# Performance work log

Hardware: AMD Instinct MI355X
Metric: run time of the kernel (lower is better)

## Reference

```python
import jax, jax.numpy as jnp
import numpy as np

N_NODES = 100000
N_EDGES = 1600000
NFEATS, NHIDS, NOUT = 128, 128, 64


def _gcn_conv(x, W, b, src, dst, n_nodes):
    # PyG GCNConv: linear transform, then symmetric-normalized aggregation
    # over A + I (self-loops added), then bias.
    h = x @ W                                        # [N, out]
    loop = jnp.arange(n_nodes, dtype=src.dtype)
    s = jnp.concatenate([src, loop])                 # [E + N]
    d = jnp.concatenate([dst, loop])                 # [E + N]
    deg = jax.ops.segment_sum(jnp.ones_like(d, dtype=h.dtype), d,
                              num_segments=n_nodes)  # degree of A + I
    dinv = jnp.where(deg > 0, jax.lax.rsqrt(deg), 0.0)
    norm = dinv[s] * dinv[d]                         # [E + N]
    msg = h[s] * norm[:, None]                       # gather + scale
    out = jax.ops.segment_sum(msg, d, num_segments=n_nodes)  # scatter-add
    return out + b


def setup_inputs() -> dict:
    key = jax.random.key(0)
    k1, k2, k3, k4 = jax.random.split(key, 4)
    edge_index = jax.random.randint(k1, (2, N_EDGES), 0, N_NODES, dtype=jnp.int64)
    x = jax.random.normal(k2, (N_NODES, NFEATS), dtype=jnp.float32)
    W1 = jax.random.normal(k3, (NFEATS, NHIDS), dtype=jnp.float32) / np.sqrt(NFEATS)
    b1 = jnp.zeros((NHIDS,), dtype=jnp.float32)
    W2 = jax.random.normal(k4, (NHIDS, NOUT), dtype=jnp.float32) / np.sqrt(NHIDS)
    b2 = jnp.zeros((NOUT,), dtype=jnp.float32)
    return {"edge_index": edge_index, "x": x, "W1": W1, "b1": b1,
            "W2": W2, "b2": b2}


def reference(edge_index, x, W1, b1, W2, b2):
    src, dst = edge_index[0], edge_index[1]
    n = x.shape[0]
    h = jax.nn.relu(_gcn_conv(x, W1, b1, src, dst, n))
    # dropout(p=0.5, train=False) is the identity in eval mode
    out = _gcn_conv(h, W2, b2, src, dst, n)
    return out
```

## Files before the change

kernel.cpp:

```cpp
#include <hip/hip_runtime.h>
#include <cstdint>
#include <cstddef>

#define NFEATS 128
#define NHIDS  128
#define NOUT   64
#define SB     256
#define CHUNK  4096

using bf16x8 = __attribute__((ext_vector_type(8))) short;
using f32x4  = __attribute__((ext_vector_type(4))) float;
using u32x4  = __attribute__((ext_vector_type(4))) unsigned int;

__device__ inline unsigned short f2bf(float f) {
    union { float f; unsigned int u; } v; v.f = f;
    unsigned int r = (v.u + 0x7FFFu + ((v.u >> 16) & 1u)) >> 16;
    return (unsigned short)r;
}
__device__ inline float bflo(unsigned int u) { return __uint_as_float(u << 16); }
__device__ inline float bfhi(unsigned int u) { return __uint_as_float(u & 0xFFFF0000u); }

__global__ void detect_wpack(const void* __restrict__ p, int* __restrict__ flag,
                             long long n_nodes,
                             const float* __restrict__ W1, unsigned short* __restrict__ Wf1,
                             const float* __restrict__ W2, unsigned short* __restrict__ Wf2) {
    if (blockIdx.x == 0) {
        if (threadIdx.x < 64) {
            const long long* q = (const long long*)p;
            long long v = q[threadIdx.x];
            int bad = (v < 0 || v >= n_nodes) ? 1 : 0;
            unsigned long long m = __ballot(bad);
            if (threadIdx.x == 0) *flag = (m != 0ULL) ? 1 : 0;
        }
        return;
    }
    int i = (blockIdx.x - 1) * 256 + threadIdx.x;
    if (i < 128 * 128) {
        int k = i >> 7, n = i & 127;
        Wf1[(((k >> 3) * 128) + n) * 8 + (k & 7)] = f2bf(W1[i]);
    }
    if (i < 128 * 64) {
        int k = i >> 6, n = i & 63;
        Wf2[(((k >> 3) * 64) + n) * 8 + (k & 7)] = f2bf(W2[i]);
    }
}

__global__ __launch_bounds__(512)
void hist_kernel(const void* __restrict__ edges, const int* __restrict__ flag,
                 int* __restrict__ histT, int ne, int nch, int nbkt) {
    __shared__ int h[1024];
    int c = blockIdx.x, t = threadIdx.x;
    for (int i = t; i < nbkt; i += 512) h[i] = 0;
    __syncthreads();
    int beg = c * CHUNK, end = min(ne, beg + CHUNK);
    bool is32 = (*flag != 0);
    for (int i = beg + t; i < end; i += 512) {
        int d = is32 ? ((const int*)edges)[ne + i]
                     : (int)((const long long*)edges)[ne + i];
        atomicAdd(&h[d >> 8], 1);
    }
    __syncthreads();
    for (int i = t; i < nbkt; i += 512)
        histT[i * nch + c] = h[i];
}

__global__ void scan_block(const int* __restrict__ v, int* __restrict__ incl,
                           int* __restrict__ partial, int n) {
    __shared__ int sh[256];
    int t = threadIdx.x;
    int i = blockIdx.x * 256 + t;
    sh[t] = (i < n) ? v[i] : 0;
    __syncthreads();
    for (int off = 1; off < 256; off <<= 1) {
        int add = (t >= off) ? sh[t - off] : 0;
        __syncthreads();
        sh[t] += add;
        __syncthreads();
    }
    if (i < n) incl[i] = sh[t];
    if (t == 255) partial[blockIdx.x] = sh[255];
}

__global__ void scan_partials(int* partial, int nb) {
    __shared__ int sh[512];
    __shared__ int carry;
    int t = threadIdx.x;
    if (t == 0) carry = 0;
    __syncthreads();
    for (int base = 0; base < nb; base += 512) {
        int idx = base + t;
        sh[t] = (idx < nb) ? partial[idx] : 0;
        __syncthreads();
        for (int off = 1; off < 512; off <<= 1) {
            int add = (t >= off) ? sh[t - off] : 0;
            __syncthreads();
            sh[t] += add;
            __syncthreads();
        }
        int excl = carry + ((t == 0) ? 0 : sh[t - 1]);
        if (idx < nb) partial[idx] = excl;
        __syncthreads();
        if (t == 0) carry += sh[511];
        __syncthreads();
    }
}

__global__ __launch_bounds__(512)
void scatter_chunks(const void* __restrict__ edges, const int* __restrict__ flag,
                    const int* __restrict__ histT, const int* __restrict__ incl,
                    const int* __restrict__ partial,
                    unsigned int* __restrict__ ebuf,
                    int ne, int nch, int nbkt) {
    __shared__ int cnt[512];
    __shared__ int cursor[512];
    __shared__ int delta[512];
    __shared__ unsigned int   srt[CHUNK];
    __shared__ unsigned short bkl[CHUNK];
    int c = blockIdx.x, t = threadIdx.x;
    if (t < nbkt) cnt[t] = 0;
    int cb = 0;
    if (t < nbkt) {
        int idx = t * nch + c;
        cb = partial[idx >> 8] + incl[idx] - histT[idx];
    }
    __syncthreads();

    int beg = c * CHUNK, end = min(ne, beg + CHUNK);
    int nloc = end - beg;
    bool is32 = (*flag != 0);

    unsigned int rec[8];
    int bk[8];
#pragma unroll
    for (int r = 0; r < 8; ++r) {
        int i = beg + t + r * 512;
        bk[r] = -1;
        if (i < end) {
            int s, d;
            if (is32) {
                s = ((const int*)edges)[i];
                d = ((const int*)edges)[ne + i];
            } else {
                s = (int)((const long long*)edges)[i];
                d = (int)((const long long*)edges)[ne + i];
            }
            rec[r] = ((unsigned int)s << 8) | (unsigned int)(d & (SB - 1));
            bk[r]  = d >> 8;
            atomicAdd(&cnt[bk[r]], 1);
        }
    }
    __syncthreads();

    int v0 = (t < nbkt) ? cnt[t] : 0;
    cursor[t] = v0;
    __syncthreads();
    for (int off = 1; off < 512; off <<= 1) {
        int add = (t >= off) ? cursor[t - off] : 0;
        __syncthreads();
        cursor[t] += add;
        __syncthreads();
    }
    int inc = cursor[t];
    __syncthreads();
    int lb = inc - v0;
    cursor[t] = lb;
    if (t < nbkt) delta[t] = cb - lb;
    __syncthreads();

#pragma unroll
    for (int r = 0; r < 8; ++r) {
        if (bk[r] >= 0) {
            int pos = atomicAdd(&cursor[bk[r]], 1);
            srt[pos] = rec[r];
            bkl[pos] = (unsigned short)bk[r];
        }
    }
    __syncthreads();

    for (int i = t; i < nloc; i += 512)
        ebuf[delta[bkl[i]] + i] = srt[i];
}

__global__ void bucket_finalize(const unsigned int* __restrict__ ebuf,
                                const int* __restrict__ histT, const int* __restrict__ inclG,
                                const int* __restrict__ partial,
                                int* __restrict__ row_ptr, float* __restrict__ dinv,
                                int* __restrict__ csr_src,
                                int n, int e, int nch, int nbkt) {
    __shared__ int deg[SB];
    __shared__ int incl[SB];
    __shared__ int cur[SB];
    __shared__ int stage[4608];
    __shared__ int sbase, sbend;
    int b = blockIdx.x, t = threadIdx.x;
    int node0 = b * SB;
    int nn = min(SB, n - node0);
    if (t == 0) {
        int i0 = b * nch;
        sbase = partial[i0 >> 8] + inclG[i0] - histT[i0];
        if (b == nbkt - 1) sbend = e;
        else {
            int i1 = (b + 1) * nch;
            sbend = partial[i1 >> 8] + inclG[i1] - histT[i1];
        }
    }
    deg[t] = 0;
    __syncthreads();
    int base = sbase, bend = sbend;

    for (int i = base + t; i < bend; i += SB)
        atomicAdd(&deg[ebuf[i] & (SB - 1)], 1);
    __syncthreads();

    incl[t] = deg[t];
    __syncthreads();
    for (int off = 1; off < SB; off <<= 1) {
        int add = (t >= off) ? incl[t - off] : 0;
        __syncthreads();
        incl[t] += add;
        __syncthreads();
    }
    int lrow = base + incl[t] - deg[t];
    cur[t] = lrow - base;
    if (t < nn) {
        row_ptr[node0 + t] = lrow;
        dinv[node0 + t]    = rsqrtf((float)(deg[t] + 1));
    }
    if (b == nbkt - 1 && t == 0) row_ptr[n] = e;
    __syncthreads();

    int cntE = bend - base;
    if (cntE <= 4608) {
        for (int i = base + t; i < bend; i += SB) {
            unsigned int r = ebuf[i];
            int pos = atomicAdd(&cur[r & (SB - 1)], 1);
            stage[pos] = (int)(r >> 8);
        }
        __syncthreads();
        for (int i = t; i < cntE; i += SB)
            csr_src[base + i] = stage[i];
    } else {
        for (int i = base + t; i < bend; i += SB) {
            unsigned int r = ebuf[i];
            int pos = atomicAdd(&cur[r & (SB - 1)], 1);
            csr_src[base + pos] = (int)(r >> 8);
        }
    }
}

template <int NC, bool F32IN>
__launch_bounds__(256)
__global__ void gemm_mfma(const void* __restrict__ Xin,
                          const unsigned short* __restrict__ Wf,
                          const float* __restrict__ dinv,
                          unsigned short* __restrict__ hs, int nrows) {
    constexpr int K = 128;
    __shared__ __align__(16) unsigned short Xl[16 * 128 * 8];

    const int tid  = threadIdx.x;
    const int row0 = blockIdx.x * 128;

    for (int i = tid; i < 128 * 32; i += 256) {
        int r  = i >> 5;
        int c4 = i & 31;
        int gr = row0 + r;
        ushort4 v = make_ushort4(0, 0, 0, 0);
        if (gr < nrows) {
            if (F32IN) {
                float4 f = ((const float4*)((const float*)Xin + (size_t)gr * K))[c4];
                v.x = f2bf(f.x); v.y = f2bf(f.y); v.z = f2bf(f.z); v.w = f2bf(f.w);
            } else {
                v = ((const ushort4*)((const unsigned short*)Xin + (size_t)gr * K))[c4];
            }
        }
        int k   = c4 * 4;
        int grp = k >> 3;
        int j0  = k & 7;
        *(ushort4*)(Xl + ((size_t)grp * 128 + r) * 8 + j0) = v;
    }
    __syncthreads();

    const int wv   = tid >> 6;
    const int lane = tid & 63;
    const int m    = lane & 15;
    const int q    = lane >> 4;

    bf16x8 af[2][4];
#pragma unroll
    for (int h = 0; h < 2; ++h)
#pragma unroll
        for (int kt = 0; kt < 4; ++kt)
            af[h][kt] = *(const bf16x8*)(Xl + (((kt * 4 + q) * 128) + h * 64 + wv * 16 + m) * 8);

    int   rbase[2];
    float dv[2][4];
#pragma unroll
    for (int h = 0; h < 2; ++h) {
        rbase[h] = row0 + h * 64 + wv * 16 + q * 4;
#pragma unroll
        for (int i = 0; i < 4; ++i)
            dv[h][i] = (rbase[h] + i < nrows) ? dinv[rbase[h] + i] : 0.f;
    }

#pragma unroll
    for (int nt = 0; nt < NC / 16; ++nt) {
        bf16x8 bfr[4];
#pragma unroll
        for (int kt = 0; kt < 4; ++kt)
            bfr[kt] = *(const bf16x8*)(Wf + (((size_t)(kt * 4 + q) * NC) + nt * 16 + m) * 8);
#pragma unroll
        for (int h = 0; h < 2; ++h) {
            f32x4 acc = {0.f, 0.f, 0.f, 0.f};
#pragma unroll
            for (int kt = 0; kt < 4; ++kt)
                acc = __builtin_amdgcn_mfma_f32_16x16x32_bf16(af[h][kt], bfr[kt], acc, 0, 0, 0);
#pragma unroll
            for (int i = 0; i < 4; ++i) {
                int g = rbase[h] + i;
                if (g < nrows)
                    hs[(size_t)g * NC + nt * 16 + m] = f2bf(acc[i] * dv[h][i]);
            }
        }
    }
}

__launch_bounds__(256)
__global__ void aggregate_fused_l1(const int* __restrict__ row_ptr,
                                   const int* __restrict__ csr_src,
                                   const uint4* __restrict__ hsu,
                                   const float* __restrict__ dinv,
                                   const float* __restrict__ b,
                                   const unsigned short* __restrict__ Wf2,
                                   unsigned short* __restrict__ hs2, int n) {
    constexpr int TPN = 16;
    constexpr int NPB = 16;
    constexpr int CH  = 16;

    __shared__ __align__(16) unsigned short h1t[16 * 136];
    __shared__ float dl[16];
    __shared__ __align__(16) unsigned short outt[16 * 64];

    const int node0 = blockIdx.x * NPB;
    const int nl    = threadIdx.x / TPN;
    const int t     = threadIdx.x % TPN;
    const int node  = min(node0 + nl, n - 1);
    const int lane  = threadIdx.x & 63;
    const int gb    = lane & ~(TPN - 1);

    uint4 u = hsu[(size_t)node * TPN + t];
    float a[8];
    a[0] = bflo(u.x); a[1] = bfhi(u.x); a[2] = bflo(u.y); a[3] = bfhi(u.y);
    a[4] = bflo(u.z); a[5] = bfhi(u.z); a[6] = bflo(u.w); a[7] = bfhi(u.w);

    int beg = row_ptr[node], end = row_ptr[node + 1];

    if (beg < end) {
        const u32x4* hb = (const u32x4*)hsu;
        u32x4 v[CH];
        int sva;
        int base = beg;

        {
            const int* pc0 = csr_src + min(base + t, end - 1);
            asm volatile("global_load_dword %0, %1, off" : "=&v"(sva) : "v"(pc0));
        }
        asm volatile("s_waitcnt vmcnt(0)");
        __builtin_amdgcn_sched_barrier(0);

        while (true) {
            int rem = min(CH, end - base);

#pragma unroll
            for (int j = 0; j < CH; ++j) {
                int jj = min(j, rem - 1);
                int sj = __shfl(sva, gb + jj, 64);
                const u32x4* p = hb + (size_t)sj * TPN + t;
                asm volatile("global_load_dwordx4 %0, %1, off" : "=&v"(v[j]) : "v"(p));
            }

            int  nbase = base + CH;
            bool more  = nbase < end;
            if (more) {
                const int* pc0 = csr_src + min(nbase + t, end - 1);
                asm volatile("global_load_dword %0, %1, off" : "=&v"(sva) : "v"(pc0));
                asm volatile("s_waitcnt vmcnt(1)");
            } else {
                asm volatile("s_waitcnt vmcnt(0)");
            }
            __builtin_amdgcn_sched_barrier(0);

#pragma unroll
            for (int j = 0; j < CH; ++j) {
                if (j < rem) {
                    unsigned int x0 = v[j][0], x1 = v[j][1], x2 = v[j][2], x3 = v[j][3];
                    a[0] += bflo(x0); a[1] += bfhi(x0);
                    a[2] += bflo(x1); a[3] += bfhi(x1);
                    a[4] += bflo(x2); a[5] += bfhi(x2);
                    a[6] += bflo(x3); a[7] += bfhi(x3);
                }
            }

            if (!more) break;
            base = nbase;
            asm volatile("s_waitcnt vmcnt(0)");
            __builtin_amdgcn_sched_barrier(0);
        }
    }

    float dvn = dinv[node];
    float4 b0 = ((const float4*)b)[2 * t];
    float4 b1 = ((const float4*)b)[2 * t + 1];
    float o[8];
    o[0] = a[0] * dvn + b0.x; o[1] = a[1] * dvn + b0.y;
    o[2] = a[2] * dvn + b0.z; o[3] = a[3] * dvn + b0.w;
    o[4] = a[4] * dvn + b1.x; o[5] = a[5] * dvn + b1.y;
    o[6] = a[6] * dvn + b1.z; o[7] = a[7] * dvn + b1.w;
#pragma unroll
    for (int j = 0; j < 8; ++j) o[j] = fmaxf(o[j], 0.f);

    uint4 ov;
    ov.x = (unsigned int)f2bf(o[0]) | ((unsigned int)f2bf(o[1]) << 16);
    ov.y = (unsigned int)f2bf(o[2]) | ((unsigned int)f2bf(o[3]) << 16);
    ov.z = (unsigned int)f2bf(o[4]) | ((unsigned int)f2bf(o[5]) << 16);
    ov.w = (unsigned int)f2bf(o[6]) | ((unsigned int)f2bf(o[7]) << 16);
    *(uint4*)((char*)h1t + (size_t)nl * 272 + t * 16) = ov;
    if (t == 0) dl[nl] = dvn;
    __syncthreads();

    {
        const int wv = threadIdx.x >> 6;
        const int m  = lane & 15;
        const int q  = lane >> 4;

        f32x4 acc = {0.f, 0.f, 0.f, 0.f};
#pragma unroll
        for (int kt = 0; kt < 4; ++kt) {
            bf16x8 af  = *(const bf16x8*)((const char*)h1t + (size_t)m * 272 + q * 16 + kt * 64);
            bf16x8 bfr = *(const bf16x8*)(Wf2 + (((size_t)(kt * 4 + q) * 64) + wv * 16 + m) * 8);
            acc = __builtin_amdgcn_mfma_f32_16x16x32_bf16(af, bfr, acc, 0, 0, 0);
        }
#pragma unroll
        for (int i = 0; i < 4; ++i) {
            int nd = q * 4 + i;
            outt[nd * 64 + wv * 16 + m] = f2bf(acc[i] * dl[nd]);
        }
    }
    __syncthreads();

    {
        int i = threadIdx.x;
        if (i < 128) {
            int gnode = node0 + (i >> 3);
            if (gnode < n)
                ((uint4*)hs2)[(size_t)gnode * 8 + (i & 7)] = ((const uint4*)outt)[i];
        }
    }
}

template <int F, bool RELU, bool OUTBF>
__launch_bounds__(256)
__global__ void aggregate_bf16(const int* __restrict__ row_ptr,
                               const int* __restrict__ csr_src,
                               const uint4* __restrict__ hsu,
                               const float* __restrict__ dinv,
                               const float* __restrict__ b,
                               void* __restrict__ out, int n) {
    constexpr int TPN  = F / 8;
    constexpr int NPB  = 256 / TPN;
    constexpr int CH   = 16;
    constexpr int NCSR = CH / TPN;
    int node = blockIdx.x * NPB + threadIdx.x / TPN;
    int t    = threadIdx.x % TPN;
    if (node >= n) return;
    const int lane = threadIdx.x & 63;
    const int gb   = lane & ~(TPN - 1);

    uint4 u = hsu[(size_t)node * TPN + t];
    float a[8];
    a[0] = bflo(u.x); a[1] = bfhi(u.x); a[2] = bflo(u.y); a[3] = bfhi(u.y);
    a[4] = bflo(u.z); a[5] = bfhi(u.z); a[6] = bflo(u.w); a[7] = bfhi(u.w);

    int beg = row_ptr[node], end = row_ptr[node + 1];

    if (beg < end) {
        const u32x4* hb = (const u32x4*)hsu;
        u32x4 v[CH];
        int sva, svb;
        int base = beg;

        {
            const int* pc0 = csr_src + min(base + t, end - 1);
            asm volatile("global_load_dword %0, %1, off" : "=&v"(sva) : "v"(pc0));
            if (NCSR == 2) {
                const int* pc1 = csr_src + min(base + TPN + t, end - 1);
                asm volatile("global_load_dword %0, %1, off" : "=&v"(svb) : "v"(pc1));
            }
        }
        asm volatile("s_waitcnt vmcnt(0)");
        __builtin_amdgcn_sched_barrier(0);

        while (true) {
            int rem = min(CH, end - base);

#pragma unroll
            for (int j = 0; j < CH; ++j) {
                int jj = min(j, rem - 1);
                int sj;
                if (TPN == 16) {
                    sj = __shfl(sva, gb + jj, 64);
                } else {
                    int s0 = __shfl(sva, gb + (jj & 7), 64);
                    int s1 = __shfl(svb, gb + (jj & 7), 64);
                    sj = (jj < 8) ? s0 : s1;
                }
                const u32x4* p = hb + (size_t)sj * TPN + t;
                asm volatile("global_load_dwordx4 %0, %1, off" : "=&v"(v[j]) : "v"(p));
            }

            int  nbase = base + CH;
            bool more  = nbase < end;
            if (more) {
                const int* pc0 = csr_src + min(nbase + t, end - 1);
                asm volatile("global_load_dword %0, %1, off" : "=&v"(sva) : "v"(pc0));
                if (NCSR == 2) {
                    const int* pc1 = csr_src + min(nbase + TPN + t, end - 1);
                    asm volatile("global_load_dword %0, %1, off" : "=&v"(svb) : "v"(pc1));
                }
                if (NCSR == 1) asm volatile("s_waitcnt vmcnt(1)");
                else           asm volatile("s_waitcnt vmcnt(2)");
            } else {
                asm volatile("s_waitcnt vmcnt(0)");
            }
            __builtin_amdgcn_sched_barrier(0);

#pragma unroll
            for (int j = 0; j < CH; ++j) {
                if (j < rem) {
                    unsigned int x0 = v[j][0], x1 = v[j][1], x2 = v[j][2], x3 = v[j][3];
                    a[0] += bflo(x0); a[1] += bfhi(x0);
                    a[2] += bflo(x1); a[3] += bfhi(x1);
                    a[4] += bflo(x2); a[5] += bfhi(x2);
                    a[6] += bflo(x3); a[7] += bfhi(x3);
                }
            }

            if (!more) break;
            base = nbase;
            asm volatile("s_waitcnt vmcnt(0)");
            __builtin_amdgcn_sched_barrier(0);
        }
    }

    float dvn = dinv[node];
    float4 b0 = ((const float4*)b)[2 * t];
    float4 b1 = ((const float4*)b)[2 * t + 1];
    float o[8];
    o[0] = a[0] * dvn + b0.x; o[1] = a[1] * dvn + b0.y;
    o[2] = a[2] * dvn + b0.z; o[3] = a[3] * dvn + b0.w;
    o[4] = a[4] * dvn + b1.x; o[5] = a[5] * dvn + b1.y;
    o[6] = a[6] * dvn + b1.z; o[7] = a[7] * dvn + b1.w;
    if (RELU) {
#pragma unroll
        for (int j = 0; j < 8; ++j) o[j] = fmaxf(o[j], 0.f);
    }
    if (OUTBF) {
        uint4 ov;
        ov.x = (unsigned int)f2bf(o[0]) | ((unsigned int)f2bf(o[1]) << 16);
        ov.y = (unsigned int)f2bf(o[2]) | ((unsigned int)f2bf(o[3]) << 16);
        ov.z = (unsigned int)f2bf(o[4]) | ((unsigned int)f2bf(o[5]) << 16);
        ov.w = (unsigned int)f2bf(o[6]) | ((unsigned int)f2bf(o[7]) << 16);
        ((uint4*)out)[(size_t)node * TPN + t] = ov;
    } else {
        float4* op = (float4*)out + (size_t)node * (F / 4) + 2 * t;
        op[0] = make_float4(o[0], o[1], o[2], o[3]);
        op[1] = make_float4(o[4], o[5], o[6], o[7]);
    }
}

extern "C" void kernel_launch(void* const* d_in, const int* in_sizes, int n_in,
                              void* d_out, int out_size, void* d_ws, size_t ws_size,
                              hipStream_t stream) {
    const void*  edge = d_in[0];
    const float* x    = (const float*)d_in[1];
    const float* W1   = (const float*)d_in[2];
    const float* b1   = (const float*)d_in[3];
    const float* W2   = (const float*)d_in[4];
    const float* b2   = (const float*)d_in[5];
    float* out = (float*)d_out;

    const int E    = in_sizes[0] / 2;
    const int N    = in_sizes[1] / NFEATS;
    const int NBKT = (N + SB - 1) / SB;
    const int NCH  = (E + CHUNK - 1) / CHUNK;
    const int M    = NBKT * NCH;

    char* w = (char*)d_ws;
    auto carve = [&](size_t bytes) { void* p = w; w += (bytes + 255) & ~(size_t)255; return p; };
    int*            flag       = (int*)           carve(256);
    int*            histT      = (int*)           carve(sizeof(int) * (size_t)M);
    int*            incl       = (int*)           carve(sizeof(int) * (size_t)M);
    int*            partial    = (int*)           carve(sizeof(int) * 4096);
    int*            row_ptr    = (int*)           carve(sizeof(int) * ((size_t)N + 1));
    float*          dinv       = (float*)         carve(sizeof(float) * (size_t)N);
    unsigned int*   ebuf       = (unsigned int*)  carve(sizeof(int) * (size_t)E);
    int*            csr_src    = (int*)           carve(sizeof(int) * (size_t)E);
    unsigned short* Wf1        = (unsigned short*)carve(2 * (size_t)NFEATS * NHIDS);
    unsigned short* Wf2        = (unsigned short*)carve(2 * (size_t)NHIDS * NOUT);
    unsigned short* hs1        = (unsigned short*)carve(2 * (size_t)N * NHIDS);
    unsigned short* hs2        = (unsigned short*)carve(2 * (size_t)N * NOUT);

    const int nbS = (M + 255) / 256;

    detect_wpack<<<65, 256, 0, stream>>>(edge, flag, (long long)N, W1, Wf1, W2, Wf2);

    hist_kernel<<<NCH, 512, 0, stream>>>(edge, flag, histT, E, NCH, NBKT);
    scan_block<<<nbS, 256, 0, stream>>>(histT, incl, partial, M);
    scan_partials<<<1, 512, 0, stream>>>(partial, nbS);
    scatter_chunks<<<NCH, 512, 0, stream>>>(edge, flag, histT, incl, partial,
                                            ebuf, E, NCH, NBKT);
    bucket_finalize<<<NBKT, SB, 0, stream>>>(ebuf, histT, incl, partial,
                                             row_ptr, dinv, csr_src, N, E, NCH, NBKT);

    gemm_mfma<NHIDS, true><<<(N + 127) / 128, 256, 0, stream>>>(x, Wf1, dinv, hs1, N);

    aggregate_fused_l1<<<(N + 15) / 16, 256, 0, stream>>>(
        row_ptr, csr_src, (const uint4*)hs1, dinv, b1, Wf2, hs2, N);

    {
        constexpr int NPB = 256 / (NOUT / 8);
        aggregate_bf16<NOUT, false, false><<<(N + NPB - 1) / NPB, 256, 0, stream>>>(
            row_ptr, csr_src, (const uint4*)hs2, dinv, b2, out, N);
    }
}
```

Baseline: 248.8 us.

## Compute degrees early and fuse layer-1 GEMM into the edge scatter launch

Degrees are now counted with global atomics in the histogram kernel, and dinv is computed alongside the partial scan. The layer-1 GEMM therefore no longer waits on bucket_finalize and runs as extra blocks of the scatter kernel, so the compute-bound GEMM can overlap the memory-bound scatter and one launch is removed. In exchange the histogram pays 1.6M global atomics on deg, and the GEMM tile is reshaped to 512-thread blocks that each handle 128 rows with one 16-row fragment per wave.

```diff
diff --git a/kernel.cpp b/kernel.cpp
--- a/kernel.cpp
+++ b/kernel.cpp
@@ -23,7 +23,8 @@
 __global__ void detect_wpack(const void* __restrict__ p, int* __restrict__ flag,
                              long long n_nodes,
                              const float* __restrict__ W1, unsigned short* __restrict__ Wf1,
-                             const float* __restrict__ W2, unsigned short* __restrict__ Wf2) {
+                             const float* __restrict__ W2, unsigned short* __restrict__ Wf2,
+                             int* __restrict__ deg, int n) {
     if (blockIdx.x == 0) {
         if (threadIdx.x < 64) {
             const long long* q = (const long long*)p;
@@ -36,18 +37,21 @@
     }
     int i = (blockIdx.x - 1) * 256 + threadIdx.x;
     if (i < 128 * 128) {
-        int k = i >> 7, n = i & 127;
-        Wf1[(((k >> 3) * 128) + n) * 8 + (k & 7)] = f2bf(W1[i]);
+        int k = i >> 7, n2 = i & 127;
+        Wf1[(((k >> 3) * 128) + n2) * 8 + (k & 7)] = f2bf(W1[i]);
     }
     if (i < 128 * 64) {
-        int k = i >> 6, n = i & 63;
-        Wf2[(((k >> 3) * 64) + n) * 8 + (k & 7)] = f2bf(W2[i]);
-    }
+        int k = i >> 6, n2 = i & 63;
+        Wf2[(((k >> 3) * 64) + n2) * 8 + (k & 7)] = f2bf(W2[i]);
+    }
+    for (int j = i; j < n; j += 64 * 256)
+        deg[j] = 0;
 }
 
 __global__ __launch_bounds__(512)
 void hist_kernel(const void* __restrict__ edges, const int* __restrict__ flag,
-                 int* __restrict__ histT, int ne, int nch, int nbkt) {
+                 int* __restrict__ histT, int* __restrict__ deg,
+                 int ne, int nch, int nbkt) {
     __shared__ int h[1024];
     int c = blockIdx.x, t = threadIdx.x;
     for (int i = t; i < nbkt; i += 512) h[i] = 0;
@@ -58,6 +62,7 @@
         int d = is32 ? ((const int*)edges)[ne + i]
                      : (int)((const long long*)edges)[ne + i];
         atomicAdd(&h[d >> 8], 1);
+        atomicAdd(&deg[d], 1);
     }
     __syncthreads();
     for (int i = t; i < nbkt; i += 512)
@@ -81,7 +86,14 @@
     if (t == 255) partial[blockIdx.x] = sh[255];
 }
 
-__global__ void scan_partials(int* partial, int nb) {
+__global__ __launch_bounds__(512)
+void scan_partials_dinv(int* __restrict__ partial, int nb,
+                        const int* __restrict__ deg, float* __restrict__ dinv, int n) {
+    if (blockIdx.x != 0) {
+        int i = (blockIdx.x - 1) * 512 + threadIdx.x;
+        if (i < n) dinv[i] = rsqrtf((float)(deg[i] + 1));
+        return;
+    }
     __shared__ int sh[512];
     __shared__ int carry;
     int t = threadIdx.x;
@@ -105,17 +117,86 @@
     }
 }
 
+__device__ __forceinline__ void gemm_tile_512(const float* __restrict__ Xin,
+                                              const unsigned short* __restrict__ Wf,
+                                              const float* __restrict__ dinv,
+                                              unsigned short* __restrict__ hs,
+                                              int nrows, int row0, char* smem) {
+    constexpr int K = 128, NC = 128;
+    unsigned short* Xl = (unsigned short*)smem;
+
+    const int tid = threadIdx.x;
+    for (int i = tid; i < 128 * 32; i += 512) {
+        int r  = i >> 5;
+        int c4 = i & 31;
+        int gr = row0 + r;
+        ushort4 v = make_ushort4(0, 0, 0, 0);
+        if (gr < nrows) {
+            float4 f = ((const float4*)(Xin + (size_t)gr * K))[c4];
+            v.x = f2bf(f.x); v.y = f2bf(f.y); v.z = f2bf(f.z); v.w = f2bf(f.w);
+        }
+        int k   = c4 * 4;
+        int grp = k >> 3;
+        int j0  = k & 7;
+        *(ushort4*)(Xl + ((size_t)grp * 128 + r) * 8 + j0) = v;
+    }
+    __syncthreads();
+
+    const int wv   = tid >> 6;
+    const int lane = tid & 63;
+    const int m    = lane & 15;
+    const int q    = lane >> 4;
+
+    bf16x8 af[4];
+#pragma unroll
+    for (int kt = 0; kt < 4; ++kt)
+        af[kt] = *(const bf16x8*)(Xl + (((kt * 4 + q) * 128) + wv * 16 + m) * 8);
+
+    const int rbase = row0 + wv * 16 + q * 4;
+    float dv[4];
+#pragma unroll
+    for (int i = 0; i < 4; ++i)
+        dv[i] = (rbase + i < nrows) ? dinv[rbase + i] : 0.f;
+
+#pragma unroll
+    for (int nt = 0; nt < NC / 16; ++nt) {
+        bf16x8 bfr[4];
+#pragma unroll
+        for (int kt = 0; kt < 4; ++kt)
+            bfr[kt] = *(const bf16x8*)(Wf + (((size_t)(kt * 4 + q) * NC) + nt * 16 + m) * 8);
+        f32x4 acc = {0.f, 0.f, 0.f, 0.f};
+#pragma unroll
+        for (int kt = 0; kt < 4; ++kt)
+            acc = __builtin_amdgcn_mfma_f32_16x16x32_bf16(af[kt], bfr[kt], acc, 0, 0, 0);
+#pragma unroll
+        for (int i = 0; i < 4; ++i) {
+            int g = rbase + i;
+            if (g < nrows)
+                hs[(size_t)g * NC + nt * 16 + m] = f2bf(acc[i] * dv[i]);
+        }
+    }
+}
+
 __global__ __launch_bounds__(512)
-void scatter_chunks(const void* __restrict__ edges, const int* __restrict__ flag,
-                    const int* __restrict__ histT, const int* __restrict__ incl,
-                    const int* __restrict__ partial,
-                    unsigned int* __restrict__ ebuf,
-                    int ne, int nch, int nbkt) {
-    __shared__ int cnt[512];
-    __shared__ int cursor[512];
-    __shared__ int delta[512];
-    __shared__ unsigned int   srt[CHUNK];
-    __shared__ unsigned short bkl[CHUNK];
+void scatter_gemm(const void* __restrict__ edges, const int* __restrict__ flag,
+                  const int* __restrict__ histT, const int* __restrict__ incl,
+                  const int* __restrict__ partial,
+                  unsigned int* __restrict__ ebuf,
+                  int ne, int nch, int nbkt,
+                  const float* __restrict__ x, const unsigned short* __restrict__ Wf1,
+                  const float* __restrict__ dinv, unsigned short* __restrict__ hs1,
+                  int nrows) {
+    __shared__ __align__(16) char smem[32768];
+    if ((int)blockIdx.x >= nch) {
+        gemm_tile_512(x, Wf1, dinv, hs1, nrows, ((int)blockIdx.x - nch) * 128, smem);
+        return;
+    }
+    int*            cnt    = (int*)smem;
+    int*            cursor = (int*)(smem + 2048);
+    int*            delta  = (int*)(smem + 4096);
+    unsigned int*   srt    = (unsigned int*)(smem + 6144);
+    unsigned short* bkl    = (unsigned short*)(smem + 22528);
+
     int c = blockIdx.x, t = threadIdx.x;
     if (t < nbkt) cnt[t] = 0;
     int cb = 0;
@@ -184,7 +265,7 @@
 __global__ void bucket_finalize(const unsigned int* __restrict__ ebuf,
                                 const int* __restrict__ histT, const int* __restrict__ inclG,
                                 const int* __restrict__ partial,
-                                int* __restrict__ row_ptr, float* __restrict__ dinv,
+                                int* __restrict__ row_ptr,
                                 int* __restrict__ csr_src,
                                 int n, int e, int nch, int nbkt) {
     __shared__ int deg[SB];
@@ -222,10 +303,7 @@
     }
     int lrow = base + incl[t] - deg[t];
     cur[t] = lrow - base;
-    if (t < nn) {
-        row_ptr[node0 + t] = lrow;
-        dinv[node0 + t]    = rsqrtf((float)(deg[t] + 1));
-    }
+    if (t < nn) row_ptr[node0 + t] = lrow;
     if (b == nbkt - 1 && t == 0) row_ptr[n] = e;
     __syncthreads();
 
@@ -244,82 +322,6 @@
             unsigned int r = ebuf[i];
             int pos = atomicAdd(&cur[r & (SB - 1)], 1);
             csr_src[base + pos] = (int)(r >> 8);
-        }
-    }
-}
-
-template <int NC, bool F32IN>
-__launch_bounds__(256)
-__global__ void gemm_mfma(const void* __restrict__ Xin,
-                          const unsigned short* __restrict__ Wf,
-                          const float* __restrict__ dinv,
-                          unsigned short* __restrict__ hs, int nrows) {
-    constexpr int K = 128;
-    __shared__ __align__(16) unsigned short Xl[16 * 128 * 8];
-
-    const int tid  = threadIdx.x;
-    const int row0 = blockIdx.x * 128;
-
-    for (int i = tid; i < 128 * 32; i += 256) {
-        int r  = i >> 5;
-        int c4 = i & 31;
-        int gr = row0 + r;
-        ushort4 v = make_ushort4(0, 0, 0, 0);
-        if (gr < nrows) {
-            if (F32IN) {
-                float4 f = ((const float4*)((const float*)Xin + (size_t)gr * K))[c4];
-                v.x = f2bf(f.x); v.y = f2bf(f.y); v.z = f2bf(f.z); v.w = f2bf(f.w);
-            } else {
-                v = ((const ushort4*)((const unsigned short*)Xin + (size_t)gr * K))[c4];
-            }
-        }
-        int k   = c4 * 4;
-        int grp = k >> 3;
-        int j0  = k & 7;
-        *(ushort4*)(Xl + ((size_t)grp * 128 + r) * 8 + j0) = v;
-    }
-    __syncthreads();
-
-    const int wv   = tid >> 6;
-    const int lane = tid & 63;
-    const int m    = lane & 15;
-    const int q    = lane >> 4;
-
-    bf16x8 af[2][4];
-#pragma unroll
-    for (int h = 0; h < 2; ++h)
-#pragma unroll
-        for (int kt = 0; kt < 4; ++kt)
-            af[h][kt] = *(const bf16x8*)(Xl + (((kt * 4 + q) * 128) + h * 64 + wv * 16 + m) * 8);
-
-    int   rbase[2];
-    float dv[2][4];
-#pragma unroll
-    for (int h = 0; h < 2; ++h) {
-        rbase[h] = row0 + h * 64 + wv * 16 + q * 4;
-#pragma unroll
-        for (int i = 0; i < 4; ++i)
-            dv[h][i] = (rbase[h] + i < nrows) ? dinv[rbase[h] + i] : 0.f;
-    }
-
-#pragma unroll
-    for (int nt = 0; nt < NC / 16; ++nt) {
-        bf16x8 bfr[4];
-#pragma unroll
-        for (int kt = 0; kt < 4; ++kt)
-            bfr[kt] = *(const bf16x8*)(Wf + (((size_t)(kt * 4 + q) * NC) + nt * 16 + m) * 8);
-#pragma unroll
-        for (int h = 0; h < 2; ++h) {
-            f32x4 acc = {0.f, 0.f, 0.f, 0.f};
-#pragma unroll
-            for (int kt = 0; kt < 4; ++kt)
-                acc = __builtin_amdgcn_mfma_f32_16x16x32_bf16(af[h][kt], bfr[kt], acc, 0, 0, 0);
-#pragma unroll
-            for (int i = 0; i < 4; ++i) {
-                int g = rbase[h] + i;
-                if (g < nrows)
-                    hs[(size_t)g * NC + nt * 16 + m] = f2bf(acc[i] * dv[h][i]);
-            }
         }
     }
 }
@@ -601,6 +603,7 @@
     int*            incl       = (int*)           carve(sizeof(int) * (size_t)M);
     int*            partial    = (int*)           carve(sizeof(int) * 4096);
     int*            row_ptr    = (int*)           carve(sizeof(int) * ((size_t)N + 1));
+    int*            deg        = (int*)           carve(sizeof(int) * (size_t)N);
     float*          dinv       = (float*)         carve(sizeof(float) * (size_t)N);
     unsigned int*   ebuf       = (unsigned int*)  carve(sizeof(int) * (size_t)E);
     int*            csr_src    = (int*)           carve(sizeof(int) * (size_t)E);
@@ -610,18 +613,23 @@
     unsigned short* hs2        = (unsigned short*)carve(2 * (size_t)N * NOUT);
 
     const int nbS = (M + 255) / 256;
-
-    detect_wpack<<<65, 256, 0, stream>>>(edge, flag, (long long)N, W1, Wf1, W2, Wf2);
-
-    hist_kernel<<<NCH, 512, 0, stream>>>(edge, flag, histT, E, NCH, NBKT);
+    const int GB  = (N + 127) / 128;
+
+    detect_wpack<<<65, 256, 0, stream>>>(edge, flag, (long long)N, W1, Wf1, W2, Wf2,
+                                         deg, N);
+
+    hist_kernel<<<NCH, 512, 0, stream>>>(edge, flag, histT, deg, E, NCH, NBKT);
+
     scan_block<<<nbS, 256, 0, stream>>>(histT, incl, partial, M);
-    scan_partials<<<1, 512, 0, stream>>>(partial, nbS);
-    scatter_chunks<<<NCH, 512, 0, stream>>>(edge, flag, histT, incl, partial,
-                                            ebuf, E, NCH, NBKT);
+    scan_partials_dinv<<<1 + (N + 511) / 512, 512, 0, stream>>>(partial, nbS,
+                                                                deg, dinv, N);
+
+    scatter_gemm<<<NCH + GB, 512, 0, stream>>>(edge, flag, histT, incl, partial,
+                                               ebuf, E, NCH, NBKT,
+                                               x, Wf1, dinv, hs1, N);
+
     bucket_finalize<<<NBKT, SB, 0, stream>>>(ebuf, histT, incl, partial,
-                                             row_ptr, dinv, csr_src, N, E, NCH, NBKT);
-
-    gemm_mfma<NHIDS, true><<<(N + 127) / 128, 256, 0, stream>>>(x, Wf1, dinv, hs1, N);
+                                             row_ptr, csr_src, N, E, NCH, NBKT);
 
     aggregate_fused_l1<<<(N + 15) / 16, 256, 0, stream>>>(
         row_ptr, csr_src, (const uint4*)hs1, dinv, b1, Wf2, hs2, N);
```

New measurement: 298.1 us. 1.2x slower.

## Store layer-2 features in feature-sliced layout and aggregate one slice per thread

Applied to the files above, without the earlier changes.

The fused layer-1 kernel now writes hs2 as 8 slices of 16 bytes per node, each stored contiguously across nodes, so slice s of node v sits at s*n+v. The layer-2 aggregation becomes a new kernel with one thread per node per slice. Each thread loads its own CSR indices and gathers 16-byte rows from a single slice, and blocks are interleaved so that consecutive blocks cover the eight slices of the same node range. The goal is to shrink the gathered working set per slice so it stays in cache, and to drop the cross-lane shuffles. In exchange, each thread now re-reads the CSR index list (eight times as many index loads) and does more serial per-thread work on high-degree nodes, which can cause imbalance within a wave.

```diff
diff --git a/kernel.cpp b/kernel.cpp
--- a/kernel.cpp
+++ b/kernel.cpp
@@ -36,12 +36,12 @@
     }
     int i = (blockIdx.x - 1) * 256 + threadIdx.x;
     if (i < 128 * 128) {
-        int k = i >> 7, n = i & 127;
-        Wf1[(((k >> 3) * 128) + n) * 8 + (k & 7)] = f2bf(W1[i]);
+        int k = i >> 7, n2 = i & 127;
+        Wf1[(((k >> 3) * 128) + n2) * 8 + (k & 7)] = f2bf(W1[i]);
     }
     if (i < 128 * 64) {
-        int k = i >> 6, n = i & 63;
-        Wf2[(((k >> 3) * 64) + n) * 8 + (k & 7)] = f2bf(W2[i]);
+        int k = i >> 6, n2 = i & 63;
+        Wf2[(((k >> 3) * 64) + n2) * 8 + (k & 7)] = f2bf(W2[i]);
     }
 }
 
@@ -450,97 +450,78 @@
     {
         int i = threadIdx.x;
         if (i < 128) {
-            int gnode = node0 + (i >> 3);
+            int sl = i >> 4;
+            int ln = i & 15;
+            int gnode = node0 + ln;
             if (gnode < n)
-                ((uint4*)hs2)[(size_t)gnode * 8 + (i & 7)] = ((const uint4*)outt)[i];
-        }
-    }
-}
-
-template <int F, bool RELU, bool OUTBF>
+                ((uint4*)hs2)[(size_t)sl * n + gnode] = ((const uint4*)outt)[ln * 8 + sl];
+        }
+    }
+}
+
 __launch_bounds__(256)
-__global__ void aggregate_bf16(const int* __restrict__ row_ptr,
-                               const int* __restrict__ csr_src,
-                               const uint4* __restrict__ hsu,
-                               const float* __restrict__ dinv,
-                               const float* __restrict__ b,
-                               void* __restrict__ out, int n) {
-    constexpr int TPN  = F / 8;
-    constexpr int NPB  = 256 / TPN;
-    constexpr int CH   = 16;
-    constexpr int NCSR = CH / TPN;
-    int node = blockIdx.x * NPB + threadIdx.x / TPN;
-    int t    = threadIdx.x % TPN;
+__global__ void aggregate_l2_sliced(const int* __restrict__ row_ptr,
+                                    const int* __restrict__ csr_src,
+                                    const uint4* __restrict__ hs2s,
+                                    const float* __restrict__ dinv,
+                                    const float* __restrict__ b,
+                                    float* __restrict__ out, int n) {
+    const int slice = blockIdx.x & 7;
+    const int node  = (blockIdx.x >> 3) * 256 + threadIdx.x;
     if (node >= n) return;
-    const int lane = threadIdx.x & 63;
-    const int gb   = lane & ~(TPN - 1);
-
-    uint4 u = hsu[(size_t)node * TPN + t];
+
+    const u32x4* hb = (const u32x4*)(hs2s + (size_t)slice * n);
+
+    u32x4 u = hb[node];
     float a[8];
-    a[0] = bflo(u.x); a[1] = bfhi(u.x); a[2] = bflo(u.y); a[3] = bfhi(u.y);
-    a[4] = bflo(u.z); a[5] = bfhi(u.z); a[6] = bflo(u.w); a[7] = bfhi(u.w);
+    a[0] = bflo(u[0]); a[1] = bfhi(u[0]); a[2] = bflo(u[1]); a[3] = bfhi(u[1]);
+    a[4] = bflo(u[2]); a[5] = bfhi(u[2]); a[6] = bflo(u[3]); a[7] = bfhi(u[3]);
 
     int beg = row_ptr[node], end = row_ptr[node + 1];
 
     if (beg < end) {
-        const u32x4* hb = (const u32x4*)hsu;
-        u32x4 v[CH];
-        int sva, svb;
+        u32x4 v[8];
+        int s[8];
         int base = beg;
 
-        {
-            const int* pc0 = csr_src + min(base + t, end - 1);
-            asm volatile("global_load_dword %0, %1, off" : "=&v"(sva) : "v"(pc0));
-            if (NCSR == 2) {
-                const int* pc1 = csr_src + min(base + TPN + t, end - 1);
-                asm volatile("global_load_dword %0, %1, off" : "=&v"(svb) : "v"(pc1));
-            }
+#pragma unroll
+        for (int j = 0; j < 8; ++j) {
+            const int* pc = csr_src + min(base + j, end - 1);
+            asm volatile("global_load_dword %0, %1, off" : "=&v"(s[j]) : "v"(pc));
         }
         asm volatile("s_waitcnt vmcnt(0)");
         __builtin_amdgcn_sched_barrier(0);
 
         while (true) {
-            int rem = min(CH, end - base);
-
-#pragma unroll
-            for (int j = 0; j < CH; ++j) {
-                int jj = min(j, rem - 1);
-                int sj;
-                if (TPN == 16) {
-                    sj = __shfl(sva, gb + jj, 64);
-                } else {
-                    int s0 = __shfl(sva, gb + (jj & 7), 64);
-                    int s1 = __shfl(svb, gb + (jj & 7), 64);
-                    sj = (jj < 8) ? s0 : s1;
-                }
-                const u32x4* p = hb + (size_t)sj * TPN + t;
+            int rem = end - base;
+
+#pragma unroll
+            for (int j = 0; j < 8; ++j) {
+                const u32x4* p = hb + s[j];
                 asm volatile("global_load_dwordx4 %0, %1, off" : "=&v"(v[j]) : "v"(p));
             }
 
-            int  nbase = base + CH;
+            int  nbase = base + 8;
             bool more  = nbase < end;
             if (more) {
-                const int* pc0 = csr_src + min(nbase + t, end - 1);
-                asm volatile("global_load_dword %0, %1, off" : "=&v"(sva) : "v"(pc0));
-                if (NCSR == 2) {
-                    const int* pc1 = csr_src + min(nbase + TPN + t, end - 1);
-                    asm volatile("global_load_dword %0, %1, off" : "=&v"(svb) : "v"(pc1));
+#pragma unroll
+                for (int j = 0; j < 8; ++j) {
+                    const int* pc = csr_src + min(nbase + j, end - 1);
+                    asm volatile("global_load_dword %0, %1, off" : "=&v"(s[j]) : "v"(pc));
                 }
-                if (NCSR == 1) asm volatile("s_waitcnt vmcnt(1)");
-                else           asm volatile("s_waitcnt vmcnt(2)");
+                asm volatile("s_waitcnt vmcnt(8)");
             } else {
                 asm volatile("s_waitcnt vmcnt(0)");
             }
             __builtin_amdgcn_sched_barrier(0);
 
 #pragma unroll
-            for (int j = 0; j < CH; ++j) {
+            for (int j = 0; j < 8; ++j) {
                 if (j < rem) {
-                    unsigned int x0 = v[j][0], x1 = v[j][1], x2 = v[j][2], x3 = v[j][3];
-                    a[0] += bflo(x0); a[1] += bfhi(x0);
-                    a[2] += bflo(x1); a[3] += bfhi(x1);
-                    a[4] += bflo(x2); a[5] += bfhi(x2);
-                    a[6] += bflo(x3); a[7] += bfhi(x3);
+                    a[0] += bflo(v[j][0]); a[1] += bfhi(v[j][0]);
+                    a[2] += bflo(v[j][1]); a[3] += bfhi(v[j][1]);
+                    a[4] += bflo(v[j][2]); a[5] += bfhi(v[j][2]);
+                    a[6] += bflo(v[j][3]); a[7] += bfhi(v[j][3]);
                 }
             }
 
@@ -552,29 +533,17 @@
     }
 
     float dvn = dinv[node];
-    float4 b0 = ((const float4*)b)[2 * t];
-    float4 b1 = ((const float4*)b)[2 * t + 1];
+    float4 b0 = ((const float4*)b)[2 * slice];
+    float4 b1 = ((const float4*)b)[2 * slice + 1];
     float o[8];
     o[0] = a[0] * dvn + b0.x; o[1] = a[1] * dvn + b0.y;
     o[2] = a[2] * dvn + b0.z; o[3] = a[3] * dvn + b0.w;
     o[4] = a[4] * dvn + b1.x; o[5] = a[5] * dvn + b1.y;
     o[6] = a[6] * dvn + b1.z; o[7] = a[7] * dvn + b1.w;
-    if (RELU) {
-#pragma unroll
-        for (int j = 0; j < 8; ++j) o[j] = fmaxf(o[j], 0.f);
-    }
-    if (OUTBF) {
-        uint4 ov;
-        ov.x = (unsigned int)f2bf(o[0]) | ((unsigned int)f2bf(o[1]) << 16);
-        ov.y = (unsigned int)f2bf(o[2]) | ((unsigned int)f2bf(o[3]) << 16);
-        ov.z = (unsigned int)f2bf(o[4]) | ((unsigned int)f2bf(o[5]) << 16);
-        ov.w = (unsigned int)f2bf(o[6]) | ((unsigned int)f2bf(o[7]) << 16);
-        ((uint4*)out)[(size_t)node * TPN + t] = ov;
-    } else {
-        float4* op = (float4*)out + (size_t)node * (F / 4) + 2 * t;
-        op[0] = make_float4(o[0], o[1], o[2], o[3]);
-        op[1] = make_float4(o[4], o[5], o[6], o[7]);
-    }
+
+    float4* op = (float4*)out + (size_t)node * (NOUT / 4) + 2 * slice;
+    op[0] = make_float4(o[0], o[1], o[2], o[3]);
+    op[1] = make_float4(o[4], o[5], o[6], o[7]);
 }
 
 extern "C" void kernel_launch(void* const* d_in, const int* in_sizes, int n_in,
@@ -627,8 +596,8 @@
         row_ptr, csr_src, (const uint4*)hs1, dinv, b1, Wf2, hs2, N);
 
     {
-        constexpr int NPB = 256 / (NOUT / 8);
-        aggregate_bf16<NOUT, false, false><<<(N + NPB - 1) / NPB, 256, 0, stream>>>(
+        int nblk = ((N + 255) / 256) * 8;
+        aggregate_l2_sliced<<<nblk, 256, 0, stream>>>(
             row_ptr, csr_src, (const uint4*)hs2, dinv, b2, out, N);
     }
 }
```

Measured after the change: 290.2 us. 16.6% more time.
